# Optimization experiments

Hardware: AMD Instinct MI355X
Metric: run time of the kernel (lower is better)

The kernel has to match this reference:

```python
import jax, jax.numpy as jnp
import numpy as np

B, D, E, H = 8192, 512, 16, 128  # batch, input_dim, num_experts, hidden_dim
EPS = 1e-5  # BatchNorm eps (torch default)


def setup_inputs() -> dict:
    key = jax.random.key(0)
    ks = iter(jax.random.split(key, 32))
    def n(shape, s=0.05):
        return jax.random.normal(next(ks), shape, dtype=jnp.float32) * s
    inp = {"x": jax.random.normal(next(ks), (B, D), dtype=jnp.float32)}
    # Router params, stacked over the 2 branches (gender, race)
    inp["rbn_gamma"] = jnp.ones((2, D), jnp.float32)
    inp["rbn_beta"] = jnp.zeros((2, D), jnp.float32)
    inp["rbn_mean"] = n((2, D))
    inp["rbn_var"] = jnp.ones((2, D), jnp.float32)
    inp["rW1"], inp["rb1"] = n((2, D, 64)), jnp.full((2, 64), 0.1, jnp.float32)
    inp["rW2"], inp["rb2"] = n((2, 64, 32)), jnp.full((2, 32), 0.1, jnp.float32)
    inp["rW3"], inp["rb3"] = n((2, 32, E)), jnp.full((2, E), 0.1, jnp.float32)
    # Expert params, stacked over [branch=2, expert=16]
    inp["ebn_gamma"] = jnp.ones((2, E, D), jnp.float32)
    inp["ebn_beta"] = jnp.zeros((2, E, D), jnp.float32)
    inp["ebn_mean"] = n((2, E, D))
    inp["ebn_var"] = jnp.ones((2, E, D), jnp.float32)
    inp["eW1"], inp["eb1"] = n((2, E, D, H)), jnp.full((2, E, H), 0.1, jnp.float32)
    inp["eW2"], inp["eb2"] = n((2, E, H, H // 2)), jnp.full((2, E, H // 2), 0.1, jnp.float32)
    inp["eW3"], inp["eb3"] = n((2, E, H // 2)), jnp.full((2, E), 0.1, jnp.float32)
    inp["branch_weights"] = jnp.array([0.5, 0.5], jnp.float32)
    return inp


def reference(x, rbn_gamma, rbn_beta, rbn_mean, rbn_var, rW1, rb1, rW2, rb2,
              rW3, rb3, ebn_gamma, ebn_beta, ebn_mean, ebn_var, eW1, eb1,
              eW2, eb2, eW3, eb3, branch_weights):
    def branch(c):
        # Router: BN(eval) -> Linear(64) -> ReLU -> Linear(32) -> ReLU -> Linear(E) -> Softmax
        xn = (x - rbn_mean[c]) * jax.lax.rsqrt(rbn_var[c] + EPS) * rbn_gamma[c] + rbn_beta[c]
        h = jax.nn.relu(xn @ rW1[c] + rb1[c])
        h = jax.nn.relu(h @ rW2[c] + rb2[c])
        rw = jax.nn.softmax(h @ rW3[c] + rb3[c], axis=1)  # [B, E]
        # Experts batched over E: per-expert BN(eval) -> Linear -> ReLU -> Linear -> ReLU -> Linear -> sigmoid
        m, v = ebn_mean[c][:, None, :], ebn_var[c][:, None, :]
        g, b = ebn_gamma[c][:, None, :], ebn_beta[c][:, None, :]
        xe = (x[None] - m) * jax.lax.rsqrt(v + EPS) * g + b          # [E, B, D]
        h1 = jax.nn.relu(jnp.einsum('ebd,edh->ebh', xe, eW1[c]) + eb1[c][:, None, :])
        h2 = jax.nn.relu(jnp.einsum('ebh,ehk->ebk', h1, eW2[c]) + eb2[c][:, None, :])
        out = jax.nn.sigmoid(jnp.einsum('ebk,ek->eb', h2, eW3[c]) + eb3[c][:, None])  # [E, B]
        return jnp.einsum('be,eb->b', rw, out)                        # weighted sum over experts
    gender_pred = branch(0)
    race_pred = branch(1)
    return branch_weights[0] * gender_pred + branch_weights[1] * race_pred
```

## Files before the change

### kernel.cpp

```cpp
#include <hip/hip_runtime.h>

typedef __attribute__((ext_vector_type(8))) short short8;
typedef __attribute__((ext_vector_type(8))) unsigned short ushort8;
typedef __attribute__((ext_vector_type(4))) float f32x4;
typedef unsigned int u32;
typedef unsigned short u16;

#define AS_GLOBAL(p) ((const __attribute__((address_space(1))) u32*)(p))
#define AS_LDS(p) ((__attribute__((address_space(3))) u32*)(p))

#define NB 8192
#define ND 512
#define NH 128

#define OFF_XPK    0u
#define OFF_W1PK   8388608u
#define OFF_W2PK   12582912u
#define OFF_RW1PT  13107200u
#define OFF_RB1P   13238272u
#define OFF_PBIAS  13238784u
#define OFF_B1P    13369856u
#define OFF_RWT    13402112u

__device__ __forceinline__ u16 f2bf(float f) {
  union { float f; u32 u; } v; v.f = f;
  return (u16)((v.u + 0x7FFFu + ((v.u >> 16) & 1u)) >> 16);
}

__global__ __launch_bounds__(256) void k_prep_all(
    const float* __restrict__ x, u16* __restrict__ xpk,
    const float* __restrict__ eg, const float* __restrict__ ebb,
    const float* __restrict__ em, const float* __restrict__ ev,
    const float* __restrict__ eW1, u16* __restrict__ w1pk, float* __restrict__ pbias,
    const float* __restrict__ eW2, u16* __restrict__ w2pk,
    const float* __restrict__ rbn_g, const float* __restrict__ rbn_b,
    const float* __restrict__ rbn_m, const float* __restrict__ rbn_v,
    const float* __restrict__ rW1, const float* __restrict__ rb1,
    u16* __restrict__ rw1pt, float* __restrict__ rb1p,
    float* __restrict__ out)
{
  __shared__ __align__(16) unsigned char sh[17920];
  const int blk = blockIdx.x, t = threadIdx.x;
  if (blk < 2048) {
    int i = (blk * 256 + t) * 8;
    const float4* p = (const float4*)(x + i);
    float4 v0 = p[0], v1 = p[1];
    ushort8 r;
    r[0] = f2bf(v0.x); r[1] = f2bf(v0.y); r[2] = f2bf(v0.z); r[3] = f2bf(v0.w);
    r[4] = f2bf(v1.x); r[5] = f2bf(v1.y); r[6] = f2bf(v1.z); r[7] = f2bf(v1.w);
    int row = i >> 9, k0 = i & 511;
    int rb = row >> 4, lr = row & 15, kb = k0 >> 5, q = (k0 >> 3) & 3;
    *(ushort8*)(xpk + ((u32)(rb * 16 + kb) * 64 + q * 16 + lr) * 8) = r;
  } else if (blk < 2304) {
    float* sa = (float*)sh;
    float* sc = sa + 64;
    u16* tile = (u16*)(sc + 64);
    float* pb2 = (float*)(tile + 64 * 128);
    const int pair = (blk - 2048) >> 3, dc = (blk - 2048) & 7;
    const int d0 = dc * 64;
    if (t < 64) {
      int d = pair * ND + d0 + t;
      float a = eg[d] * rsqrtf(ev[d] + 1e-5f);
      sa[t] = a;
      sc[t] = ebb[d] - em[d] * a;
    }
    __syncthreads();
    const int h = t & 127, pr = t >> 7;
    float acc = 0.f;
    const float* src = eW1 + (size_t)pair * ND * NH + (size_t)d0 * NH;
#pragma unroll
    for (int i = 0; i < 32; ++i) {
      int dl = i * 2 + pr;
      float w = src[dl * NH + h];
      tile[dl * 128 + h] = f2bf(w * sa[dl]);
      acc += w * sc[dl];
    }
    pb2[pr * 128 + h] = acc;
    __syncthreads();
    {
      int hh = t >> 1, half = t & 1;
      const int nb = hh >> 4, lr = hh & 15;
#pragma unroll
      for (int v8 = 0; v8 < 4; ++v8) {
        int db = d0 + half * 32 + v8 * 8;
        int kb = db >> 5, q = (db >> 3) & 3;
        ushort8 r;
#pragma unroll
        for (int j = 0; j < 8; ++j) r[j] = tile[(half * 32 + v8 * 8 + j) * 128 + hh];
        *(ushort8*)(w1pk + (u32)((pair * 16 + kb) * 8 + nb) * 512 + (q * 16 + lr) * 8) = r;
      }
    }
    if (t < 128) pbias[(u32)(pair * 8 + dc) * 128 + t] = pb2[t] + pb2[128 + t];
  } else if (blk < 2336) {
    const int pair = blk - 2304;
    const float* w2 = eW2 + (size_t)pair * NH * 64;
    int n = t & 63, kk = t >> 6;
    for (int k = kk * 32; k < kk * 32 + 32; ++k) {
      u32 dst = ((u32)((pair * 4 + (k >> 5)) * 4 + (n >> 4))) * 512
              + (((k >> 3) & 3) * 16 + (n & 15)) * 8 + (k & 7);
      w2pk[dst] = f2bf(w2[k * 64 + n]);
    }
  } else if (blk < 2338) {
    const int c = blk - 2336;
    int n = t >> 2, q = t & 3;
    const float* g  = rbn_g + c * ND;
    const float* b  = rbn_b + c * ND;
    const float* m  = rbn_m + c * ND;
    const float* vv = rbn_v + c * ND;
    const float* w1 = rW1 + (size_t)c * ND * 64;
    float acc = 0.f;
    for (int d = q * 128; d < q * 128 + 128; ++d) {
      float a  = g[d] * rsqrtf(vv[d] + 1e-5f);
      float cc = b[d] - m[d] * a;
      float w  = w1[d * 64 + n];
      rw1pt[((u32)c * 64 + n) * ND + d] = f2bf(a * w);
      acc += cc * w;
    }
    acc += __shfl_xor(acc, 1, 64);
    acc += __shfl_xor(acc, 2, 64);
    if (q == 0) rb1p[c * 64 + n] = rb1[c * 64 + n] + acc;
  } else {
    float4 z; z.x = 0.f; z.y = 0.f; z.z = 0.f; z.w = 0.f;
    float4* o4 = (float4*)out;
#pragma unroll
    for (int j = 0; j < 8; ++j) o4[t * 8 + j] = z;
  }
}

__global__ __launch_bounds__(256) void k_router(
    const u16* __restrict__ xpk, const u16* __restrict__ rw1pt,
    const float* __restrict__ rb1p, const float* __restrict__ rW2,
    const float* __restrict__ rb2, const float* __restrict__ rW3,
    const float* __restrict__ rb3, float* __restrict__ rwT,
    const float* __restrict__ pbias, const float* __restrict__ eb1,
    float* __restrict__ b1p)
{
  __shared__ float h1l[64][65];
  __shared__ float h2l[64][33];
  __shared__ float w2s[2048];
  __shared__ float w3s[512];
  const int tid = threadIdx.x;
  if (blockIdx.x >= 256) {
    const int pair = blockIdx.x - 256;
    if (tid < 128) {
      float s = eb1[pair * NH + tid];
#pragma unroll
      for (int dc = 0; dc < 8; ++dc) s += pbias[(u32)(pair * 8 + dc) * 128 + tid];
      b1p[pair * NH + tid] = s;
    }
    return;
  }
  const int lane = tid & 63;
  const int wv = tid >> 6;
  const int q = lane >> 4;
  const int lr = lane & 15;
  const int c = blockIdx.x >> 7;
  const int r0 = (blockIdx.x & 127) * 64;
  {
    const float* W2 = rW2 + c * 2048;
    *(float4*)(w2s + tid * 8)     = *(const float4*)(W2 + tid * 8);
    *(float4*)(w2s + tid * 8 + 4) = *(const float4*)(W2 + tid * 8 + 4);
    if (tid < 128)
      *(float4*)(w3s + tid * 4) = *(const float4*)(rW3 + c * 512 + tid * 4);
  }
  f32x4 acc[4] = {};
  const u16* xfr   = xpk + ((u32)((r0 >> 4) + wv) * 16) * 512 + (u32)lane * 8;
  const u16* wbase = rw1pt + ((u32)c * 64 << 9);
  for (int kb = 0; kb < 16; ++kb) {
    short8 a = *(const short8*)(xfr + kb * 512);
#pragma unroll
    for (int u = 0; u < 4; ++u) {
      short8 b = *(const short8*)(wbase + (((u32)(u * 16 + lr)) << 9) + kb * 32 + q * 8);
      acc[u] = __builtin_amdgcn_mfma_f32_16x16x32_bf16(a, b, acc[u], 0, 0, 0);
    }
  }
#pragma unroll
  for (int u = 0; u < 4; ++u) {
    int n = u * 16 + lr;
    float bias = rb1p[c * 64 + n];
#pragma unroll
    for (int i = 0; i < 4; ++i) {
      float v = acc[u][i] + bias;
      h1l[wv * 16 + q * 4 + i][n] = v > 0.f ? v : 0.f;
    }
  }
  __syncthreads();
  {
    int row = tid >> 2, part = (tid & 3) * 8;
    float hv[8];
#pragma unroll
    for (int j = 0; j < 8; ++j) hv[j] = rb2[c * 32 + part + j];
#pragma unroll
    for (int k = 0; k < 64; ++k) {
      float hk = h1l[row][k];
#pragma unroll
      for (int j = 0; j < 8; ++j) hv[j] += hk * w2s[k * 32 + part + j];
    }
#pragma unroll
    for (int j = 0; j < 8; ++j) h2l[row][part + j] = hv[j] > 0.f ? hv[j] : 0.f;
  }
  __syncthreads();
  {
    int row = tid >> 2, e0 = (tid & 3) * 4;
    float lg[4];
#pragma unroll
    for (int e = 0; e < 4; ++e) {
      float a3 = rb3[c * 16 + e0 + e];
#pragma unroll
      for (int k = 0; k < 32; ++k) a3 += h2l[row][k] * w3s[k * 16 + e0 + e];
      lg[e] = a3;
    }
    float mx = fmaxf(fmaxf(lg[0], lg[1]), fmaxf(lg[2], lg[3]));
    mx = fmaxf(mx, __shfl_xor(mx, 1, 64));
    mx = fmaxf(mx, __shfl_xor(mx, 2, 64));
    float sm = 0.f;
#pragma unroll
    for (int e = 0; e < 4; ++e) { lg[e] = __expf(lg[e] - mx); sm += lg[e]; }
    sm += __shfl_xor(sm, 1, 64);
    sm += __shfl_xor(sm, 2, 64);
    float inv = 1.f / sm;
#pragma unroll
    for (int e = 0; e < 4; ++e)
      rwT[(u32)(c * 16 + e0 + e) * NB + r0 + row] = lg[e] * inv;
  }
}

__global__ __launch_bounds__(256, 2) void k_expert(
    const u16* __restrict__ xpk, const float* __restrict__ b1p,
    const u16* __restrict__ w2pk,
    const float* __restrict__ eb2, const float* __restrict__ eW3,
    const float* __restrict__ eb3, const float* __restrict__ rwT,
    const float* __restrict__ bw, float* __restrict__ out)
{
  extern __shared__ __align__(16) unsigned char smem[];
  const int tid = threadIdx.x;
  const int lane = tid & 63;
  const int wv = tid >> 6;
  const int q = lane >> 4, lr = lane & 15;
  const int wr = wv >> 1;
  const int p  = wv & 1;
  const int xcd  = blockIdx.x & 7;
  const int slot = blockIdx.x >> 3;
  const int pt   = xcd * 2 + (slot & 1);
  const int bt   = slot >> 1;
  const int pr0  = pt * 2;
  const int r0   = bt * 128;
  const u32 lane16 = (u32)lane * 16;

  u32 soff[6], sstep[6], slds[6];
#pragma unroll
  for (int j = 0; j < 6; ++j) {
    int f = wv * 6 + j;
    if (f < 8) {
      soff[j]  = ((u32)(bt * 8 + f) * 16) * 512 + (u32)lane * 8;
      sstep[j] = 512;
      slds[j]  = (u32)f * 1024;
    } else {
      int g = f - 8;
      soff[j]  = 4194304u + ((u32)(pr0 + (g >> 3)) * 128 + (g & 7)) * 512 + (u32)lane * 8;
      sstep[j] = 4096;
      slds[j]  = 8192 + (u32)g * 1024;
    }
  }

#define STAGE(BUF, KB) do { \
  _Pragma("unroll") for (int j_ = 0; j_ < 6; ++j_) \
    __builtin_amdgcn_global_load_lds( \
        AS_GLOBAL(xpk + soff[j_] + (u32)(KB) * sstep[j_]), \
        AS_LDS(smem + (BUF) + slds[j_]), 16, 0, 0); \
  } while (0)

  f32x4 acc[4][8] = {};

  STAGE(0u, 0);
  STAGE(24576u, 1);
  asm volatile("s_waitcnt vmcnt(6)" ::: "memory");
  __builtin_amdgcn_s_barrier();

#pragma unroll
  for (int kb = 0; kb < 16; ++kb) {
    const u32 BUF = (u32)(kb % 3) * 24576u;
    if (kb < 14) {
      STAGE((u32)((kb + 2) % 3) * 24576u, kb + 2);
      __builtin_amdgcn_sched_barrier(0);
    }
    short8 a_[4], b_[8];
#pragma unroll
    for (int t = 0; t < 4; ++t)
      a_[t] = *(const short8*)(smem + BUF + (u32)(wr * 4 + t) * 1024 + lane16);
#pragma unroll
    for (int u = 0; u < 8; ++u)
      b_[u] = *(const short8*)(smem + BUF + 8192 + (u32)(p * 8 + u) * 1024 + lane16);
#pragma unroll
    for (int t = 0; t < 4; ++t)
#pragma unroll
      for (int u = 0; u < 8; ++u)
        acc[t][u] = __builtin_amdgcn_mfma_f32_16x16x32_bf16(a_[t], b_[u], acc[t][u], 0, 0, 0);
    if (kb < 14)       asm volatile("s_waitcnt vmcnt(6)" ::: "memory");
    else if (kb == 14) asm volatile("s_waitcnt vmcnt(0)" ::: "memory");
    if (kb < 15) __builtin_amdgcn_s_barrier();
  }
#undef STAGE

  __syncthreads();

  {
    float b1w[8];
#pragma unroll
    for (int u = 0; u < 8; ++u) b1w[u] = b1p[(pr0 + p) * NH + u * 16 + lr];
#pragma unroll
    for (int t = 0; t < 4; ++t)
#pragma unroll
      for (int u = 0; u < 8; ++u) {
        const int rb = wr * 4 + t;
        const int kb2 = u >> 1;
        const int q2 = (u & 1) * 2 + (lr >> 3), j2 = lr & 7;
#pragma unroll
        for (int i = 0; i < 4; ++i) {
          float v = acc[t][u][i] + b1w[u];
          v = v > 0.f ? v : 0.f;
          u32 byteoff = ((u32)(((p * 8 + rb) * 4 + kb2) * 64 + q2 * 16 + q * 4 + i)) * 16 + j2 * 2;
          *(u16*)(smem + byteoff) = f2bf(v);
        }
      }
  }
  __syncthreads();

  f32x4 acc2[2][2][4] = {};
#pragma unroll
  for (int pl = 0; pl < 2; ++pl)
#pragma unroll
    for (int kk = 0; kk < 4; ++kk) {
      short8 a2[2], b2[4];
#pragma unroll
      for (int t2 = 0; t2 < 2; ++t2)
        a2[t2] = *(const short8*)(smem + (u32)(((pl * 8 + wv * 2 + t2) * 4 + kk)) * 1024 + lane16);
#pragma unroll
      for (int u2 = 0; u2 < 4; ++u2)
        b2[u2] = *(const short8*)(w2pk + ((u32)(((pr0 + pl) * 4 + kk) * 4 + u2)) * 512 + (u32)lane * 8);
#pragma unroll
      for (int t2 = 0; t2 < 2; ++t2)
#pragma unroll
        for (int u2 = 0; u2 < 4; ++u2)
          acc2[pl][t2][u2] = __builtin_amdgcn_mfma_f32_16x16x32_bf16(a2[t2], b2[u2], acc2[pl][t2][u2], 0, 0, 0);
    }

#pragma unroll
  for (int pl = 0; pl < 2; ++pl) {
    const int pairG = pr0 + pl;
    float bb2[4], bw3v[4];
#pragma unroll
    for (int u2 = 0; u2 < 4; ++u2) {
      bb2[u2]  = eb2[pairG * 64 + u2 * 16 + lr];
      bw3v[u2] = eW3[pairG * 64 + u2 * 16 + lr];
    }
    float b3 = eb3[pairG];
    float bwc = bw[pairG >> 4];
#pragma unroll
    for (int t2 = 0; t2 < 2; ++t2) {
      float pp[4] = {0.f, 0.f, 0.f, 0.f};
#pragma unroll
      for (int u2 = 0; u2 < 4; ++u2)
#pragma unroll
        for (int i = 0; i < 4; ++i) {
          float h = acc2[pl][t2][u2][i] + bb2[u2];
          h = h > 0.f ? h : 0.f;
          pp[i] += h * bw3v[u2];
        }
#pragma unroll
      for (int m = 1; m < 16; m <<= 1)
#pragma unroll
        for (int i = 0; i < 4; ++i) pp[i] += __shfl_xor(pp[i], m, 64);
      if (lr == 0) {
#pragma unroll
        for (int i = 0; i < 4; ++i) {
          int row = wv * 32 + t2 * 16 + q * 4 + i;
          float z = pp[i] + b3;
          float s = 1.f / (1.f + __expf(-z));
          float rw = rwT[(u32)pairG * NB + r0 + row];
          atomicAdd(out + r0 + row, bwc * rw * s);
        }
      }
    }
  }
}

extern "C" void kernel_launch(void* const* d_in, const int* in_sizes, int n_in,
                              void* d_out, int out_size, void* d_ws, size_t ws_size,
                              hipStream_t stream) {
  const float* x     = (const float*)d_in[0];
  const float* rbn_g = (const float*)d_in[1];
  const float* rbn_b = (const float*)d_in[2];
  const float* rbn_m = (const float*)d_in[3];
  const float* rbn_v = (const float*)d_in[4];
  const float* rW1   = (const float*)d_in[5];
  const float* rb1   = (const float*)d_in[6];
  const float* rW2   = (const float*)d_in[7];
  const float* rb2   = (const float*)d_in[8];
  const float* rW3   = (const float*)d_in[9];
  const float* rb3   = (const float*)d_in[10];
  const float* ebn_g = (const float*)d_in[11];
  const float* ebn_b = (const float*)d_in[12];
  const float* ebn_m = (const float*)d_in[13];
  const float* ebn_v = (const float*)d_in[14];
  const float* eW1   = (const float*)d_in[15];
  const float* eb1   = (const float*)d_in[16];
  const float* eW2   = (const float*)d_in[17];
  const float* eb2   = (const float*)d_in[18];
  const float* eW3   = (const float*)d_in[19];
  const float* eb3   = (const float*)d_in[20];
  const float* bw    = (const float*)d_in[21];

  char* ws = (char*)d_ws;
  u16*   xpk   = (u16*)(ws + OFF_XPK);
  u16*   w1pk  = (u16*)(ws + OFF_W1PK);
  u16*   w2pk  = (u16*)(ws + OFF_W2PK);
  u16*   rw1pt = (u16*)(ws + OFF_RW1PT);
  float* rb1p  = (float*)(ws + OFF_RB1P);
  float* pbias = (float*)(ws + OFF_PBIAS);
  float* b1p   = (float*)(ws + OFF_B1P);
  float* rwT   = (float*)(ws + OFF_RWT);
  float* outf  = (float*)d_out;

  k_prep_all<<<dim3(2339), dim3(256), 0, stream>>>(
      x, xpk, ebn_g, ebn_b, ebn_m, ebn_v, eW1, w1pk, pbias, eW2, w2pk,
      rbn_g, rbn_b, rbn_m, rbn_v, rW1, rb1, rw1pt, rb1p, outf);
  k_router<<<dim3(288), dim3(256), 0, stream>>>(
      xpk, rw1pt, rb1p, rW2, rb2, rW3, rb3, rwT, pbias, eb1, b1p);
  k_expert<<<dim3(1024), dim3(256), 73728, stream>>>(
      xpk, b1p, w2pk, eb2, eW3, eb3, rwT, bw, outf);
}
```

Measured before the change: 89.68 us.

## Interleave LDS fragment reads with MFMA clusters and prefetch next k-block A tiles

Restructures the main GEMM k-loop so the B-fragment LDS reads are split into pairs interleaved with 8-MFMA clusters, using explicit lgkmcnt waits and sched_barriers. The A fragments and the first B pair for the next k-block are prefetched into double-buffered registers after the barrier, before the last MFMA cluster runs. s_setprio is raised around the MFMA clusters. The aim is to hide LDS latency behind matrix math instead of loading every fragment up front, at the cost of more registers and fragile hand-written wait counts.

```diff
diff --git a/kernel.cpp b/kernel.cpp
--- a/kernel.cpp
+++ b/kernel.cpp
@@ -269,38 +269,60 @@
         AS_GLOBAL(xpk + soff[j_] + (u32)(KB) * sstep[j_]), \
         AS_LDS(smem + (BUF) + slds[j_]), 16, 0, 0); \
   } while (0)
+#define SB __builtin_amdgcn_sched_barrier(0)
+#define RDA(KB, T) (*(const short8*)(smem + (u32)((KB) % 3) * 24576u + (u32)(wr * 4 + (T)) * 1024 + lane16))
+#define RDB(KB, U) (*(const short8*)(smem + (u32)((KB) % 3) * 24576u + 8192 + (u32)(p * 8 + (U)) * 1024 + lane16))
+#define CLUSTER(C, U0, BX, BY) do { \
+  __builtin_amdgcn_s_setprio(1); \
+  _Pragma("unroll") for (int t_ = 0; t_ < 4; ++t_) { \
+    acc[t_][U0]     = __builtin_amdgcn_mfma_f32_16x16x32_bf16(aR[C][t_], BX, acc[t_][U0], 0, 0, 0); \
+    acc[t_][U0 + 1] = __builtin_amdgcn_mfma_f32_16x16x32_bf16(aR[C][t_], BY, acc[t_][U0 + 1], 0, 0, 0); \
+  } \
+  __builtin_amdgcn_s_setprio(0); \
+  } while (0)
 
   f32x4 acc[4][8] = {};
+  short8 aR[2][4];
+  short8 b0, b1, b2, b3, b4, b5, b6, b7;
 
   STAGE(0u, 0);
   STAGE(24576u, 1);
   asm volatile("s_waitcnt vmcnt(6)" ::: "memory");
   __builtin_amdgcn_s_barrier();
+  aR[0][0] = RDA(0, 0); aR[0][1] = RDA(0, 1); aR[0][2] = RDA(0, 2); aR[0][3] = RDA(0, 3);
+  b0 = RDB(0, 0); b1 = RDB(0, 1);
 
 #pragma unroll
   for (int kb = 0; kb < 16; ++kb) {
-    const u32 BUF = (u32)(kb % 3) * 24576u;
-    if (kb < 14) {
-      STAGE((u32)((kb + 2) % 3) * 24576u, kb + 2);
-      __builtin_amdgcn_sched_barrier(0);
-    }
-    short8 a_[4], b_[8];
-#pragma unroll
-    for (int t = 0; t < 4; ++t)
-      a_[t] = *(const short8*)(smem + BUF + (u32)(wr * 4 + t) * 1024 + lane16);
-#pragma unroll
-    for (int u = 0; u < 8; ++u)
-      b_[u] = *(const short8*)(smem + BUF + 8192 + (u32)(p * 8 + u) * 1024 + lane16);
-#pragma unroll
-    for (int t = 0; t < 4; ++t)
-#pragma unroll
-      for (int u = 0; u < 8; ++u)
-        acc[t][u] = __builtin_amdgcn_mfma_f32_16x16x32_bf16(a_[t], b_[u], acc[t][u], 0, 0, 0);
-    if (kb < 14)       asm volatile("s_waitcnt vmcnt(6)" ::: "memory");
-    else if (kb == 14) asm volatile("s_waitcnt vmcnt(0)" ::: "memory");
+    const int c = kb & 1, n = c ^ 1;
+    b2 = RDB(kb, 2); b3 = RDB(kb, 3);
+    if (kb < 14) STAGE((u32)((kb + 2) % 3) * 24576u, kb + 2);
+    asm volatile("s_waitcnt lgkmcnt(2)" ::: "memory"); SB;
+    CLUSTER(c, 0, b0, b1); SB;
+    b4 = RDB(kb, 4); b5 = RDB(kb, 5);
+    asm volatile("s_waitcnt lgkmcnt(2)" ::: "memory"); SB;
+    CLUSTER(c, 2, b2, b3); SB;
+    b6 = RDB(kb, 6); b7 = RDB(kb, 7);
+    asm volatile("s_waitcnt lgkmcnt(2)" ::: "memory"); SB;
+    CLUSTER(c, 4, b4, b5); SB;
+    if (kb < 14) asm volatile("s_waitcnt vmcnt(6)" ::: "memory");
+    else         asm volatile("s_waitcnt vmcnt(0)" ::: "memory");
+    __builtin_amdgcn_s_barrier();
+    if (kb < 15) {
+      aR[n][0] = RDA(kb + 1, 0); aR[n][1] = RDA(kb + 1, 1);
+      aR[n][2] = RDA(kb + 1, 2); aR[n][3] = RDA(kb + 1, 3);
+      b0 = RDB(kb + 1, 0); b1 = RDB(kb + 1, 1);
+      asm volatile("s_waitcnt lgkmcnt(6)" ::: "memory"); SB;
+    } else {
+      asm volatile("s_waitcnt lgkmcnt(0)" ::: "memory"); SB;
+    }
+    CLUSTER(c, 6, b6, b7); SB;
     if (kb < 15) __builtin_amdgcn_s_barrier();
   }
 #undef STAGE
+#undef RDA
+#undef RDB
+#undef CLUSTER
 
   __syncthreads();
 
@@ -331,18 +353,18 @@
   for (int pl = 0; pl < 2; ++pl)
 #pragma unroll
     for (int kk = 0; kk < 4; ++kk) {
-      short8 a2[2], b2[4];
+      short8 a2[2], b2v[4];
 #pragma unroll
       for (int t2 = 0; t2 < 2; ++t2)
         a2[t2] = *(const short8*)(smem + (u32)(((pl * 8 + wv * 2 + t2) * 4 + kk)) * 1024 + lane16);
 #pragma unroll
       for (int u2 = 0; u2 < 4; ++u2)
-        b2[u2] = *(const short8*)(w2pk + ((u32)(((pr0 + pl) * 4 + kk) * 4 + u2)) * 512 + (u32)lane * 8);
+        b2v[u2] = *(const short8*)(w2pk + ((u32)(((pr0 + pl) * 4 + kk) * 4 + u2)) * 512 + (u32)lane * 8);
 #pragma unroll
       for (int t2 = 0; t2 < 2; ++t2)
 #pragma unroll
         for (int u2 = 0; u2 < 4; ++u2)
-          acc2[pl][t2][u2] = __builtin_amdgcn_mfma_f32_16x16x32_bf16(a2[t2], b2[u2], acc2[pl][t2][u2], 0, 0, 0);
+          acc2[pl][t2][u2] = __builtin_amdgcn_mfma_f32_16x16x32_bf16(a2[t2], b2v[u2], acc2[pl][t2][u2], 0, 0, 0);
     }
 
 #pragma unroll
```

Measured after the change: 89.36 us. Within noise of the previous version (-0.3%).
